# Kernel tuning notes

Hardware: AMD Instinct MI355X
Metric: run time of the kernel (lower is better)

Reference implementation:

```python
import jax, jax.numpy as jnp
import numpy as np

H = 8          # num_heads
WIN = 256      # window_size (even); half-window = 128
NEG = -1e30    # stand-in for -inf that keeps softmax grad finite


def setup_inputs() -> dict:
    key = jax.random.key(0)
    ks = jax.random.split(key, 6)
    B, S, D, E = 2, 2048, 512, 512
    x = jax.random.normal(ks[0], (B, S, D), dtype=jnp.float32)
    padding_mask = jax.random.randint(ks[1], (B, S), 0, 2, dtype=jnp.int32)
    Wqkv = jax.random.normal(ks[2], (3 * E, D), dtype=jnp.float32) * 0.02
    bqkv = jnp.zeros((3 * E,), dtype=jnp.float32)
    Wo = jax.random.normal(ks[3], (E, E), dtype=jnp.float32) * 0.02
    bo = jnp.zeros((E,), dtype=jnp.float32)
    return {"x": x, "padding_mask": padding_mask, "Wqkv": Wqkv, "bqkv": bqkv,
            "Wo": Wo, "bo": bo}


def reference(x, padding_mask, Wqkv, bqkv, Wo, bo):
    B, S, _ = x.shape
    E = Wo.shape[0]
    Dh = E // H
    # qkv projection -> [B, H, S, 3*Dh]
    qkv = (x @ Wqkv.T + bqkv).reshape(B, S, H, 3 * Dh).transpose(0, 2, 1, 3)
    q, k, v = jnp.split(qkv, 3, axis=-1)
    # full S x S scores (original materializes [B,H,S,S]); scale by sqrt(head_dim)
    scores = jnp.einsum('bhsd,bhtd->bhst', q, k) / jnp.sqrt(jnp.float32(Dh))
    # sliding-window band: |i - j| <= window_size // 2
    i = jnp.arange(S)[:, None]
    j = jnp.arange(S)[None, :]
    band = jnp.abs(i - j) <= (WIN // 2)               # [S, S]
    # padding: entry valid only if both row and col tokens are non-pad
    pad = padding_mask.astype(bool)                    # [B, S]
    valid = band[None, None] & pad[:, None, None, :] & pad[:, None, :, None]
    scores = jnp.where(valid, scores, NEG)
    A = jax.nn.softmax(scores, axis=-1)
    # rows with no valid entry -> nan_to_num(., 0) in original -> zeros here
    row_valid = jnp.any(valid, axis=-1, keepdims=True)
    A = jnp.where(row_valid, A, 0.0)
    Y = jnp.einsum('bhst,bhtd->bhsd', A, v)            # [B,H,S,Dh]
    Y = Y.transpose(0, 2, 1, 3).reshape(B, S, E)
    return Y @ Wo.T + bo
```

## Files before the change

### kernel.cpp

```cpp
#include <hip/hip_runtime.h>

#define NH   8
#define SEQ  2048
#define DIM  512
#define EMB  512
#define DH   64
#define HALF 128
#define QT   16
#define KW   272
#define SCS  276

typedef __attribute__((ext_vector_type(8))) short short8;
typedef __attribute__((ext_vector_type(4))) float f32x4;

__device__ __forceinline__ unsigned short f2bf(float f) {
    unsigned int u = __float_as_uint(f);
    return (unsigned short)((u + 0x7fffu + ((u >> 16) & 1u)) >> 16);
}

__device__ __forceinline__ void gload_lds16(const void* g, void* l) {
    __builtin_amdgcn_global_load_lds((__attribute__((address_space(1))) void*)g,
                                     (__attribute__((address_space(3))) void*)l,
                                     16, 0, 0);
}

__global__ __launch_bounds__(256)
void cvt_all(const float* __restrict__ x, const float* __restrict__ wqkv,
             const float* __restrict__ wo, unsigned short* __restrict__ out) {
    const int i = blockIdx.x * 256 + threadIdx.x;
    const float* src;
    int base;
    if (i < 524288)      { src = x;    base = 0; }
    else if (i < 720896) { src = wqkv; base = 524288; }
    else                 { src = wo;   base = 720896; }
    float4 v = ((const float4*)src)[i - base];
    ((ushort4*)out)[i] = make_ushort4(f2bf(v.x), f2bf(v.y), f2bf(v.z), f2bf(v.w));
}

__global__ __launch_bounds__(256)
void gemm_qkv(const unsigned short* __restrict__ A, const unsigned short* __restrict__ B,
              const float* __restrict__ bias, unsigned short* __restrict__ qkvh,
              unsigned short* __restrict__ vT) {
    constexpr int BM = 128, BN = 64, BK = 32;
    const int K = DIM;
    __shared__ unsigned short As[BM * BK];
    __shared__ unsigned short Bs[BN * BK];
    const int t = threadIdx.x, lane = t & 63, wid = t >> 6;
    const int wr = wid >> 1, wc = wid & 1;
    const int bm = blockIdx.y * BM, bn = blockIdx.x * BN;

    f32x4 acc[4][2];
    #pragma unroll
    for (int m = 0; m < 4; ++m)
        #pragma unroll
        for (int n = 0; n < 2; ++n)
            acc[m][n] = (f32x4){0.f, 0.f, 0.f, 0.f};

    const int lr = lane & 15, lg = lane >> 4, lk = lg * 8;
    for (int kt = 0; kt < K; kt += BK) {
        #pragma unroll
        for (int off = 0; off < BM * BK; off += 2048) {
            const int e = off + t * 8, r = e >> 5, c = e & 31;
            gload_lds16(A + (size_t)(bm + r) * K + kt + c, &As[e]);
        }
        {
            const int e = t * 8, r = e >> 5, c = e & 31;
            gload_lds16(B + (size_t)(bn + r) * K + kt + c, &Bs[e]);
        }
        __syncthreads();
        short8 af[4], bf[2];
        #pragma unroll
        for (int m = 0; m < 4; ++m) af[m] = *(const short8*)&As[(wr * 64 + m * 16 + lr) * BK + lk];
        #pragma unroll
        for (int n = 0; n < 2; ++n) bf[n] = *(const short8*)&Bs[(wc * 32 + n * 16 + lr) * BK + lk];
        #pragma unroll
        for (int m = 0; m < 4; ++m)
            #pragma unroll
            for (int n = 0; n < 2; ++n)
                acc[m][n] = __builtin_amdgcn_mfma_f32_16x16x32_bf16(af[m], bf[n], acc[m][n], 0, 0, 0);
        __syncthreads();
    }

    const int bb = bm >> 11;
    const int sbase = (bm & 2047) + wr * 64 + lg * 4;
    const int oc0 = bn + wc * 32 + lr;
    #pragma unroll
    for (int n = 0; n < 2; ++n) {
        const int col = oc0 + n * 16;
        const int h = col / 192, rem = col - h * 192;
        const int ty = rem >> 6, d = rem & 63;
        const float bv = bias[col];
        if (ty == 2) {
            unsigned short* vrow = vT + ((size_t)(bb * NH + h) * DH + d) * SEQ;
            #pragma unroll
            for (int m = 0; m < 4; ++m) {
                const int s0 = sbase + m * 16;
                ushort4 pk = make_ushort4(f2bf(acc[m][n][0] + bv), f2bf(acc[m][n][1] + bv),
                                          f2bf(acc[m][n][2] + bv), f2bf(acc[m][n][3] + bv));
                *(ushort4*)&vrow[s0] = pk;
            }
        } else {
            unsigned short* plane = qkvh + (((size_t)(bb * NH + h) * 3 + ty) * SEQ) * DH + d;
            #pragma unroll
            for (int m = 0; m < 4; ++m)
                #pragma unroll
                for (int r = 0; r < 4; ++r)
                    plane[(size_t)(sbase + m * 16 + r) * DH] = f2bf(acc[m][n][r] + bv);
        }
    }
}

template<int BM, int BN, int WR, int WC>
__global__ __launch_bounds__(256)
void gemm_bf16(const unsigned short* __restrict__ A, const unsigned short* __restrict__ B,
               const float* __restrict__ bias, float* __restrict__ C,
               int M, int N, int K) {
    constexpr int BK = 32;
    constexpr int WM = BM / WR, WN = BN / WC;
    constexpr int FM = WM / 16, FN = WN / 16;
    __shared__ unsigned short As[BM * BK];
    __shared__ unsigned short Bs[BN * BK];
    const int t = threadIdx.x, lane = t & 63, wid = t >> 6;
    const int wr = wid / WC, wc = wid % WC;
    const int bm = blockIdx.y * BM, bn = blockIdx.x * BN;

    f32x4 acc[FM][FN];
    #pragma unroll
    for (int m = 0; m < FM; ++m)
        #pragma unroll
        for (int n = 0; n < FN; ++n)
            acc[m][n] = (f32x4){0.f, 0.f, 0.f, 0.f};

    const int lr = lane & 15, lk = (lane >> 4) * 8;
    for (int kt = 0; kt < K; kt += BK) {
        #pragma unroll
        for (int off = 0; off < BM * BK; off += 2048) {
            const int e = off + t * 8, r = e >> 5, c = e & 31;
            gload_lds16(A + (size_t)(bm + r) * K + kt + c, &As[e]);
        }
        #pragma unroll
        for (int off = 0; off < BN * BK; off += 2048) {
            const int e = off + t * 8, r = e >> 5, c = e & 31;
            gload_lds16(B + (size_t)(bn + r) * K + kt + c, &Bs[e]);
        }
        __syncthreads();
        short8 af[FM], bf[FN];
        #pragma unroll
        for (int m = 0; m < FM; ++m) af[m] = *(const short8*)&As[(wr * WM + m * 16 + lr) * BK + lk];
        #pragma unroll
        for (int n = 0; n < FN; ++n) bf[n] = *(const short8*)&Bs[(wc * WN + n * 16 + lr) * BK + lk];
        #pragma unroll
        for (int m = 0; m < FM; ++m)
            #pragma unroll
            for (int n = 0; n < FN; ++n)
                acc[m][n] = __builtin_amdgcn_mfma_f32_16x16x32_bf16(af[m], bf[n], acc[m][n], 0, 0, 0);
        __syncthreads();
    }

    const int orow = bm + wr * WM + (lane >> 4) * 4;
    const int oc0 = bn + wc * WN + (lane & 15);
    #pragma unroll
    for (int m = 0; m < FM; ++m)
        #pragma unroll
        for (int n = 0; n < FN; ++n) {
            const int col = oc0 + n * 16;
            const float bv = bias[col];
            #pragma unroll
            for (int r = 0; r < 4; ++r)
                C[(size_t)(orow + m * 16 + r) * N + col] = acc[m][n][r] + bv;
        }
}

__global__ __launch_bounds__(256)
void attn_mfma(const unsigned short* __restrict__ qkvh,
               const unsigned short* __restrict__ vT,
               const int* __restrict__ pad,
               unsigned short* __restrict__ Yb) {
    const int bh = blockIdx.y, b = bh >> 3, h = bh & 7;
    const int i0 = blockIdx.x * QT, kb = i0 - HALF;
    const int t = threadIdx.x, lane = t & 63, w = t >> 6;
    const int lr = lane & 15, lg = lane >> 4;

    __shared__ float Sc[QT * SCS];

    const unsigned short* Qg = qkvh + ((size_t)bh * 3 + 0) * SEQ * DH;
    const unsigned short* Kg = qkvh + ((size_t)bh * 3 + 1) * SEQ * DH;
    const unsigned short* vTg = vT + (size_t)bh * DH * SEQ;
    const int* padb = pad + b * SEQ;

    short8 qf[2];
    #pragma unroll
    for (int kk = 0; kk < 2; ++kk)
        qf[kk] = *(const short8*)&Qg[(size_t)(i0 + lr) * DH + kk * 32 + lg * 8];

    const int k0 = w * 16;
    #pragma unroll
    for (int c = 0; c < 5; ++c) {
        const int nc = (c < 4) ? 64 : 16;
        if (k0 < nc) {
            const int jl = c * 64 + k0 + lr;
            const int j = kb + jl;
            const int jc = j < 0 ? 0 : (j > SEQ - 1 ? SEQ - 1 : j);
            const int kv = (j >= 0 && j < SEQ) ? padb[j] : 0;
            f32x4 a0 = (f32x4){0.f, 0.f, 0.f, 0.f};
            #pragma unroll
            for (int kk = 0; kk < 2; ++kk) {
                const short8 bfr = *(const short8*)&Kg[(size_t)jc * DH + kk * 32 + lg * 8];
                a0 = __builtin_amdgcn_mfma_f32_16x16x32_bf16(qf[kk], bfr, a0, 0, 0, 0);
            }
            #pragma unroll
            for (int r = 0; r < 4; ++r) {
                const int q0 = lg * 4 + r;
                const bool ok = kv && (jl >= q0) && (jl <= q0 + 2 * HALF);
                Sc[q0 * SCS + jl] = ok ? a0[r] * 0.125f : -1e30f;
            }
        }
    }
    __syncthreads();

    for (int r = w; r < QT; r += 4) {
        float* row = &Sc[r * SCS];
        unsigned short* prow = (unsigned short*)row;
        if (!padb[i0 + r]) {
            #pragma unroll
            for (int u = 0; u < 5; ++u) {
                const int jl = lane + 64 * u;
                if (jl < KW) prow[jl] = 0;
            }
            if (lane >= 16 && lane < 32) prow[256 + lane] = 0;
            continue;
        }
        float v[5];
        float mx = -1e30f;
        #pragma unroll
        for (int u = 0; u < 5; ++u) {
            const int jl = lane + 64 * u;
            v[u] = (jl < KW) ? row[jl] : -1e30f;
            mx = fmaxf(mx, v[u]);
        }
        #pragma unroll
        for (int off = 32; off; off >>= 1) mx = fmaxf(mx, __shfl_xor(mx, off));
        float s = 0.f;
        #pragma unroll
        for (int u = 0; u < 5; ++u) { v[u] = __expf(v[u] - mx); s += v[u]; }
        #pragma unroll
        for (int off = 32; off; off >>= 1) s += __shfl_xor(s, off);
        const float inv = 1.f / s;
        asm volatile("" ::: "memory");
        #pragma unroll
        for (int u = 0; u < 5; ++u) {
            const int jl = lane + 64 * u;
            if (jl < KW) prow[jl] = f2bf(v[u] * inv);
        }
        if (lane >= 16 && lane < 32) prow[256 + lane] = 0;
    }
    __syncthreads();

    f32x4 o0 = (f32x4){0.f, 0.f, 0.f, 0.f};
    const unsigned short* PbU = (const unsigned short*)Sc;
    const int d0 = w * 16 + lr;
    #pragma unroll
    for (int c = 0; c < 5; ++c) {
        const int nkk = (c < 4) ? 2 : 1;
        #pragma unroll
        for (int kk = 0; kk < nkk; ++kk) {
            int j0 = kb + c * 64 + kk * 32 + lg * 8;
            j0 = j0 < 0 ? 0 : (j0 > SEQ - 8 ? SEQ - 8 : j0);
            const short8 vf = *(const short8*)&vTg[(size_t)d0 * SEQ + j0];
            const short8 pf = *(const short8*)&PbU[lr * (SCS * 2) + c * 64 + kk * 32 + lg * 8];
            o0 = __builtin_amdgcn_mfma_f32_16x16x32_bf16(pf, vf, o0, 0, 0, 0);
        }
    }

    #pragma unroll
    for (int r = 0; r < 4; ++r)
        Yb[(size_t)(b * SEQ + i0 + lg * 4 + r) * EMB + h * DH + d0] = f2bf(o0[r]);
}

extern "C" void kernel_launch(void* const* d_in, const int* in_sizes, int n_in,
                              void* d_out, int out_size, void* d_ws, size_t ws_size,
                              hipStream_t stream) {
    const float* x    = (const float*)d_in[0];
    const int*   pad  = (const int*)d_in[1];
    const float* Wqkv = (const float*)d_in[2];
    const float* bqkv = (const float*)d_in[3];
    const float* Wo   = (const float*)d_in[4];
    const float* bo   = (const float*)d_in[5];
    float* out = (float*)d_out;

    const int BS = 2 * SEQ;
    char* p = (char*)d_ws;
    unsigned short* qkvh  = (unsigned short*)p;
    unsigned short* vT    = (unsigned short*)(p + 12582912);
    unsigned short* xb    = (unsigned short*)(p + 16777216);
    unsigned short* wqkvb = (unsigned short*)(p + 20971520);
    unsigned short* wob   = (unsigned short*)(p + 22544384);
    unsigned short* Yb    = xb;

    dim3 blk(256);
    cvt_all<<<dim3(3072), blk, 0, stream>>>(x, Wqkv, Wo, xb);
    gemm_qkv<<<dim3(24, 32), blk, 0, stream>>>(xb, wqkvb, bqkv, qkvh, vT);
    attn_mfma<<<dim3(SEQ / QT, 2 * NH), blk, 0, stream>>>(qkvh, vT, pad, Yb);
    gemm_bf16<64, 64, 2, 2><<<dim3(EMB / 64, BS / 64), blk, 0, stream>>>(
        Yb, wob, bo, out, BS, EMB, DIM);
}
```

Before: 59.87 us.

## Use BK=64 with XOR-swizzled LDS and staged coalesced QKV epilogue

Both GEMMs move from a K-tile of 32 to 64 and store LDS tiles with an XOR swizzle on 16-byte chunks, which halves the number of barriers per K and is meant to cut LDS bank conflicts on the MFMA fragment reads. The QKV GEMM epilogue now stages the bias-added bf16 tile in shared memory and then writes Q/K planes and the transposed V with 16-byte vector stores, replacing scattered 2-byte strided stores. In exchange it uses more shared memory per block and adds an extra barrier and LDS round-trip in the epilogue.

After: 58.38 us. 1.03x faster.

```diff
diff --git a/kernel.cpp b/kernel.cpp
--- a/kernel.cpp
+++ b/kernel.cpp
@@ -41,13 +41,14 @@
 void gemm_qkv(const unsigned short* __restrict__ A, const unsigned short* __restrict__ B,
               const float* __restrict__ bias, unsigned short* __restrict__ qkvh,
               unsigned short* __restrict__ vT) {
-    constexpr int BM = 128, BN = 64, BK = 32;
-    const int K = DIM;
-    __shared__ unsigned short As[BM * BK];
-    __shared__ unsigned short Bs[BN * BK];
+    constexpr int BM = 128, BN = 64, BK = 64;
+    __shared__ unsigned short SM[BM * BK + BN * BK];
+    unsigned short* As = SM;
+    unsigned short* Bs = SM + BM * BK;
     const int t = threadIdx.x, lane = t & 63, wid = t >> 6;
     const int wr = wid >> 1, wc = wid & 1;
     const int bm = blockIdx.y * BM, bn = blockIdx.x * BN;
+    const int lr = lane & 15, lg = lane >> 4;
 
     f32x4 acc[4][2];
     #pragma unroll
@@ -56,73 +57,93 @@
         for (int n = 0; n < 2; ++n)
             acc[m][n] = (f32x4){0.f, 0.f, 0.f, 0.f};
 
-    const int lr = lane & 15, lg = lane >> 4, lk = lg * 8;
-    for (int kt = 0; kt < K; kt += BK) {
+    for (int kt = 0; kt < DIM; kt += BK) {
         #pragma unroll
         for (int off = 0; off < BM * BK; off += 2048) {
-            const int e = off + t * 8, r = e >> 5, c = e & 31;
-            gload_lds16(A + (size_t)(bm + r) * K + kt + c, &As[e]);
-        }
-        {
-            const int e = t * 8, r = e >> 5, c = e & 31;
-            gload_lds16(B + (size_t)(bn + r) * K + kt + c, &Bs[e]);
+            const int e = off + t * 8, r = e >> 6, c4 = (e & 63) >> 3;
+            const int gc = (c4 ^ (r & 7)) << 3;
+            gload_lds16(A + (size_t)(bm + r) * DIM + kt + gc, &As[e]);
+        }
+        #pragma unroll
+        for (int off = 0; off < BN * BK; off += 2048) {
+            const int e = off + t * 8, r = e >> 6, c4 = (e & 63) >> 3;
+            const int gc = (c4 ^ (r & 7)) << 3;
+            gload_lds16(B + (size_t)(bn + r) * DIM + kt + gc, &Bs[e]);
         }
         __syncthreads();
-        short8 af[4], bf[2];
-        #pragma unroll
-        for (int m = 0; m < 4; ++m) af[m] = *(const short8*)&As[(wr * 64 + m * 16 + lr) * BK + lk];
-        #pragma unroll
-        for (int n = 0; n < 2; ++n) bf[n] = *(const short8*)&Bs[(wc * 32 + n * 16 + lr) * BK + lk];
-        #pragma unroll
-        for (int m = 0; m < 4; ++m)
-            #pragma unroll
-            for (int n = 0; n < 2; ++n)
-                acc[m][n] = __builtin_amdgcn_mfma_f32_16x16x32_bf16(af[m], bf[n], acc[m][n], 0, 0, 0);
-        __syncthreads();
-    }
-
-    const int bb = bm >> 11;
-    const int sbase = (bm & 2047) + wr * 64 + lg * 4;
-    const int oc0 = bn + wc * 32 + lr;
-    #pragma unroll
-    for (int n = 0; n < 2; ++n) {
-        const int col = oc0 + n * 16;
-        const int h = col / 192, rem = col - h * 192;
-        const int ty = rem >> 6, d = rem & 63;
-        const float bv = bias[col];
-        if (ty == 2) {
-            unsigned short* vrow = vT + ((size_t)(bb * NH + h) * DH + d) * SEQ;
+        short8 af[2][4], bf[2][2];
+        #pragma unroll
+        for (int kk = 0; kk < 2; ++kk) {
             #pragma unroll
             for (int m = 0; m < 4; ++m) {
-                const int s0 = sbase + m * 16;
-                ushort4 pk = make_ushort4(f2bf(acc[m][n][0] + bv), f2bf(acc[m][n][1] + bv),
-                                          f2bf(acc[m][n][2] + bv), f2bf(acc[m][n][3] + bv));
-                *(ushort4*)&vrow[s0] = pk;
-            }
-        } else {
-            unsigned short* plane = qkvh + (((size_t)(bb * NH + h) * 3 + ty) * SEQ) * DH + d;
+                const int row = wr * 64 + m * 16 + lr;
+                af[kk][m] = *(const short8*)&As[row * 64 + (((kk * 4 + lg) ^ (row & 7)) << 3)];
+            }
+            #pragma unroll
+            for (int n = 0; n < 2; ++n) {
+                const int row = wc * 32 + n * 16 + lr;
+                bf[kk][n] = *(const short8*)&Bs[row * 64 + (((kk * 4 + lg) ^ (row & 7)) << 3)];
+            }
+        }
+        #pragma unroll
+        for (int kk = 0; kk < 2; ++kk)
             #pragma unroll
             for (int m = 0; m < 4; ++m)
                 #pragma unroll
-                for (int r = 0; r < 4; ++r)
-                    plane[(size_t)(sbase + m * 16 + r) * DH] = f2bf(acc[m][n][r] + bv);
-        }
-    }
-}
-
-template<int BM, int BN, int WR, int WC>
+                for (int n = 0; n < 2; ++n)
+                    acc[m][n] = __builtin_amdgcn_mfma_f32_16x16x32_bf16(af[kk][m], bf[kk][n], acc[m][n], 0, 0, 0);
+        __syncthreads();
+    }
+
+    unsigned short* Tr = SM;
+    #pragma unroll
+    for (int n = 0; n < 2; ++n) {
+        const int cl = wc * 32 + n * 16 + lr;
+        const float bv = bias[bn + cl];
+        #pragma unroll
+        for (int m = 0; m < 4; ++m)
+            #pragma unroll
+            for (int r = 0; r < 4; ++r)
+                Tr[(wr * 64 + m * 16 + lg * 4 + r) * 72 + cl] = f2bf(acc[m][n][r] + bv);
+    }
+    __syncthreads();
+
+    const int h = bn / 192, ty = (bn >> 6) % 3;
+    const int bb = bm >> 11, s0 = bm & 2047;
+    if (ty < 2) {
+        unsigned short* plane = qkvh + (((size_t)(bb * NH + h) * 3 + ty) * SEQ) * DH;
+        const int s = t >> 1, hf = (t & 1) * 32;
+        unsigned short* dst = plane + (size_t)(s0 + s) * DH + hf;
+        #pragma unroll
+        for (int k8 = 0; k8 < 4; ++k8)
+            *(short8*)&dst[k8 * 8] = *(const short8*)&Tr[s * 72 + hf + k8 * 8];
+    } else {
+        const int d = t >> 2, p = t & 3;
+        unsigned short* vrow = vT + ((size_t)(bb * NH + h) * DH + d) * SEQ + s0 + p * 32;
+        #pragma unroll
+        for (int k8 = 0; k8 < 4; ++k8) {
+            alignas(16) unsigned short tmp[8];
+            #pragma unroll
+            for (int k = 0; k < 8; ++k) tmp[k] = Tr[(p * 32 + k8 * 8 + k) * 72 + d];
+            *(short8*)&vrow[k8 * 8] = *(short8*)tmp;
+        }
+    }
+}
+
+template<int BM, int BN, int BK, int WR, int WC>
 __global__ __launch_bounds__(256)
 void gemm_bf16(const unsigned short* __restrict__ A, const unsigned short* __restrict__ B,
                const float* __restrict__ bias, float* __restrict__ C,
                int M, int N, int K) {
-    constexpr int BK = 32;
     constexpr int WM = BM / WR, WN = BN / WC;
     constexpr int FM = WM / 16, FN = WN / 16;
+    constexpr int KK = BK / 32;
     __shared__ unsigned short As[BM * BK];
     __shared__ unsigned short Bs[BN * BK];
     const int t = threadIdx.x, lane = t & 63, wid = t >> 6;
     const int wr = wid / WC, wc = wid % WC;
     const int bm = blockIdx.y * BM, bn = blockIdx.x * BN;
+    const int lr = lane & 15, lg = lane >> 4;
 
     f32x4 acc[FM][FN];
     #pragma unroll
@@ -131,34 +152,46 @@
         for (int n = 0; n < FN; ++n)
             acc[m][n] = (f32x4){0.f, 0.f, 0.f, 0.f};
 
-    const int lr = lane & 15, lk = (lane >> 4) * 8;
     for (int kt = 0; kt < K; kt += BK) {
         #pragma unroll
         for (int off = 0; off < BM * BK; off += 2048) {
-            const int e = off + t * 8, r = e >> 5, c = e & 31;
-            gload_lds16(A + (size_t)(bm + r) * K + kt + c, &As[e]);
+            const int e = off + t * 8, r = e >> 6, c4 = (e & 63) >> 3;
+            const int gc = (c4 ^ (r & 7)) << 3;
+            gload_lds16(A + (size_t)(bm + r) * K + kt + gc, &As[e]);
         }
         #pragma unroll
         for (int off = 0; off < BN * BK; off += 2048) {
-            const int e = off + t * 8, r = e >> 5, c = e & 31;
-            gload_lds16(B + (size_t)(bn + r) * K + kt + c, &Bs[e]);
+            const int e = off + t * 8, r = e >> 6, c4 = (e & 63) >> 3;
+            const int gc = (c4 ^ (r & 7)) << 3;
+            gload_lds16(B + (size_t)(bn + r) * K + kt + gc, &Bs[e]);
         }
         __syncthreads();
-        short8 af[FM], bf[FN];
-        #pragma unroll
-        for (int m = 0; m < FM; ++m) af[m] = *(const short8*)&As[(wr * WM + m * 16 + lr) * BK + lk];
-        #pragma unroll
-        for (int n = 0; n < FN; ++n) bf[n] = *(const short8*)&Bs[(wc * WN + n * 16 + lr) * BK + lk];
-        #pragma unroll
-        for (int m = 0; m < FM; ++m)
-            #pragma unroll
-            for (int n = 0; n < FN; ++n)
-                acc[m][n] = __builtin_amdgcn_mfma_f32_16x16x32_bf16(af[m], bf[n], acc[m][n], 0, 0, 0);
+        short8 af[KK][FM], bf[KK][FN];
+        #pragma unroll
+        for (int kk = 0; kk < KK; ++kk) {
+            #pragma unroll
+            for (int m = 0; m < FM; ++m) {
+                const int row = wr * WM + m * 16 + lr;
+                af[kk][m] = *(const short8*)&As[row * BK + (((kk * 4 + lg) ^ (row & 7)) << 3)];
+            }
+            #pragma unroll
+            for (int n = 0; n < FN; ++n) {
+                const int row = wc * WN + n * 16 + lr;
+                bf[kk][n] = *(const short8*)&Bs[row * BK + (((kk * 4 + lg) ^ (row & 7)) << 3)];
+            }
+        }
+        #pragma unroll
+        for (int kk = 0; kk < KK; ++kk)
+            #pragma unroll
+            for (int m = 0; m < FM; ++m)
+                #pragma unroll
+                for (int n = 0; n < FN; ++n)
+                    acc[m][n] = __builtin_amdgcn_mfma_f32_16x16x32_bf16(af[kk][m], bf[kk][n], acc[m][n], 0, 0, 0);
         __syncthreads();
     }
 
-    const int orow = bm + wr * WM + (lane >> 4) * 4;
-    const int oc0 = bn + wc * WN + (lane & 15);
+    const int orow = bm + wr * WM + lg * 4;
+    const int oc0 = bn + wc * WN + lr;
     #pragma unroll
     for (int m = 0; m < FM; ++m)
         #pragma unroll
@@ -301,6 +334,6 @@
     cvt_all<<<dim3(3072), blk, 0, stream>>>(x, Wqkv, Wo, xb);
     gemm_qkv<<<dim3(24, 32), blk, 0, stream>>>(xb, wqkvb, bqkv, qkvh, vT);
     attn_mfma<<<dim3(SEQ / QT, 2 * NH), blk, 0, stream>>>(qkvh, vT, pad, Yb);
-    gemm_bf16<64, 64, 2, 2><<<dim3(EMB / 64, BS / 64), blk, 0, stream>>>(
+    gemm_bf16<64, 64, 64, 2, 2><<<dim3(EMB / 64, BS / 64), blk, 0, stream>>>(
         Yb, wob, bo, out, BS, EMB, DIM);
 }
```
